# Kernel tuning notes

Hardware: AMD Instinct MI355X
Metric: run time of the kernel (lower is better)

The kernel has to match this reference:

```python
import jax, jax.numpy as jnp
import numpy as np

BETA = 0.25

def setup_inputs() -> dict:
    key = jax.random.key(0)
    k1, k2 = jax.random.split(key)
    x = jax.random.normal(k1, (16, 32, 32, 256), dtype=jnp.float32)
    embed = jax.random.normal(k2, (256, 8192), dtype=jnp.float32)
    return {"x": x, "embed": embed}

def reference(x, embed):
    dim = embed.shape[0]
    flatten = x.reshape(-1, dim)  # [N, dim]
    # squared L2 distance to each code: ||f||^2 - 2 f.e + ||e||^2 -> [N, n_embed]
    dist = (jnp.sum(flatten * flatten, axis=1, keepdims=True)
            - 2.0 * (flatten @ embed)
            + jnp.sum(embed * embed, axis=0, keepdims=True))
    ind = jnp.argmin(dist, axis=1)  # == argmax(-dist)
    embed_ind = ind.reshape(x.shape[:-1])  # [B, H, W]
    codebook = embed.T  # [n_embed, dim]
    quantize = codebook[embed_ind]  # gather -> [B, H, W, dim]
    diff = jnp.mean((jax.lax.stop_gradient(quantize) - x) ** 2)
    commit_loss = jnp.mean((quantize - jax.lax.stop_gradient(x)) ** 2)
    diff = diff + commit_loss * BETA
    quantize = x + jax.lax.stop_gradient(quantize - x)  # straight-through
    return quantize, diff, embed_ind
```

## Files before the change

kernel.cpp:

```cpp
#include <hip/hip_runtime.h>

static constexpr int DIM   = 256;
static constexpr int NCODE = 8192;
static constexpr int NROWS = 16384;

typedef __bf16 bf16x8 __attribute__((ext_vector_type(8)));
typedef float  f32x4  __attribute__((ext_vector_type(4)));

__device__ __forceinline__ void top2_insert(float& v0, int& i0, float& v1, int& i1,
                                            float s, int si) {
    if (s < v0) { v1 = v0; i1 = i0; v0 = s; i0 = si; }
    else if (s < v1) { v1 = s; i1 = si; }
}
__device__ __forceinline__ void top2_merge(float& v0, int& i0, float& v1, int& i1,
                                           float b0, int bi0, float b1, int bi1) {
    if (b0 < v0) {
        if (b1 < v0) { v0 = b0; i0 = bi0; v1 = b1; i1 = bi1; }
        else         { v1 = v0; i1 = i0;  v0 = b0; i0 = bi0; }
    } else if (b0 < v1) { v1 = b0; i1 = bi0; }
}

__global__ __launch_bounds__(256) void prep_kernel(
    const float* __restrict__ x, const float* __restrict__ embed,
    ushort* __restrict__ xb, ushort* __restrict__ eb16,
    float* __restrict__ ebT32, float* __restrict__ e2)
{
    __shared__ float tile[64][65];
    const int b = blockIdx.x;
    const int t = threadIdx.x;

    if (b < 2048) {
        int i = b * 256 + t;
        const float4* xp = (const float4*)x + (size_t)i * 2;
        float4 a = xp[0], v = xp[1];
        bf16x8 o;
        o[0] = (__bf16)a.x; o[1] = (__bf16)a.y; o[2] = (__bf16)a.z; o[3] = (__bf16)a.w;
        o[4] = (__bf16)v.x; o[5] = (__bf16)v.y; o[6] = (__bf16)v.z; o[7] = (__bf16)v.w;
        ((bf16x8*)xb)[i] = o;
    } else if (b < 2560) {
        const int eb = b - 2048;
        const int c00 = (eb & 127) * 64;
        const int k0  = (eb >> 7) * 64;
        const int tc  = t & 63, tr4 = t >> 6;
        #pragma unroll
        for (int i = 0; i < 16; ++i) {
            int r = i * 4 + tr4;
            tile[r][tc] = embed[(size_t)(k0 + r) * NCODE + c00 + tc];
        }
        __syncthreads();
        const int cl = t >> 2;
        const int kq = t & 3;
        float vals[16];
        #pragma unroll
        for (int j = 0; j < 16; ++j) vals[j] = tile[kq * 16 + j][cl];
        float* d32 = ebT32 + (size_t)(c00 + cl) * DIM + k0 + kq * 16;
        #pragma unroll
        for (int j = 0; j < 4; ++j)
            *(float4*)(d32 + j * 4) = make_float4(vals[j*4], vals[j*4+1],
                                                  vals[j*4+2], vals[j*4+3]);
        bf16x8 h0, h1;
        #pragma unroll
        for (int j = 0; j < 8; ++j) { h0[j] = (__bf16)vals[j]; h1[j] = (__bf16)vals[8 + j]; }
        ushort* d16 = eb16 + (size_t)(c00 + cl) * DIM + k0 + kq * 16;
        *(bf16x8*)d16 = h0;
        *(bf16x8*)(d16 + 8) = h1;
    } else {
        int j = (b - 2560) * 256 + t;
        float s = 0.f;
        for (int k = 0; k < DIM; ++k) {
            float v = embed[(size_t)k * NCODE + j];
            s = __fadd_rn(s, __fmul_rn(v, v));
        }
        e2[j] = s;
    }
}

__global__ __launch_bounds__(512, 1) void gemm_top2_kernel(
    const ushort* __restrict__ xb,
    const ushort* __restrict__ eb,
    const float* __restrict__ e2g,
    uint2* __restrict__ scratch)
{
    __shared__ ushort Bs[32768];
    __shared__ ushort As[2][16384];
    __shared__ uint4  ldsM[4][64];

    const int t     = threadIdx.x;
    const int chunk = blockIdx.x >> 2;
    const int rg    = blockIdx.x & 3;
    const int c0    = chunk * 128;
    const int rowbase = rg * 4096;

    const int wid = t >> 6, lane = t & 63;
    const int wr  = wid >> 2, wc = wid & 3;
    const int lr  = lane & 15, g = lane >> 4;

    {
        const char* bb = (const char*)(eb + (size_t)c0 * DIM);
        uint4 breg[8];
        #pragma unroll
        for (int i = 0; i < 8; ++i)
            breg[i] = *(const uint4*)(bb + i * 8192 + t * 16);
        #pragma unroll
        for (int i = 0; i < 8; ++i) {
            int o = i * 8192 + t * 16;
            int row = o >> 9, col = o & 511;
            *(uint4*)((char*)Bs + row * 512 + (col ^ ((row & 7) << 4))) = breg[i];
        }
        const char* ab = (const char*)(xb + (size_t)rowbase * DIM);
        uint4 areg[4];
        #pragma unroll
        for (int i = 0; i < 4; ++i)
            areg[i] = *(const uint4*)(ab + i * 8192 + t * 16);
        #pragma unroll
        for (int i = 0; i < 4; ++i) {
            int o = i * 8192 + t * 16;
            int row = o >> 9, col = o & 511;
            *(uint4*)((char*)As[0] + row * 512 + (col ^ ((row & 7) << 4))) = areg[i];
        }
    }
    __syncthreads();

    float e2v[2];
    #pragma unroll
    for (int fc = 0; fc < 2; ++fc) e2v[fc] = e2g[c0 + wc * 32 + fc * 16 + lr];

    int cur = 0;
    for (int tt = 0; tt < 64; ++tt) {
        uint4 areg[4];
        if (tt < 63) {
            const char* ab = (const char*)(xb + (size_t)(rowbase + (tt + 1) * 64) * DIM);
            #pragma unroll
            for (int i = 0; i < 4; ++i)
                areg[i] = *(const uint4*)(ab + i * 8192 + t * 16);
        }

        f32x4 acc[2][2];
        #pragma unroll
        for (int a = 0; a < 2; ++a)
            #pragma unroll
            for (int b2 = 0; b2 < 2; ++b2) acc[a][b2] = (f32x4){0.f, 0.f, 0.f, 0.f};

        const char* Ab = (const char*)As[cur];
        const char* Bb = (const char*)Bs;
        #pragma unroll
        for (int ks = 0; ks < 8; ++ks) {
            bf16x8 af[2], bfr[2];
            #pragma unroll
            for (int fr = 0; fr < 2; ++fr) {
                int row = wr * 32 + fr * 16 + lr;
                int col = (ks * 64 + g * 16) ^ ((row & 7) << 4);
                af[fr] = *(const bf16x8*)(Ab + row * 512 + col);
            }
            #pragma unroll
            for (int fc = 0; fc < 2; ++fc) {
                int code = wc * 32 + fc * 16 + lr;
                int col  = (ks * 64 + g * 16) ^ ((code & 7) << 4);
                bfr[fc] = *(const bf16x8*)(Bb + code * 512 + col);
            }
            #pragma unroll
            for (int fr = 0; fr < 2; ++fr)
                #pragma unroll
                for (int fc = 0; fc < 2; ++fc)
                    acc[fr][fc] = __builtin_amdgcn_mfma_f32_16x16x32_bf16(
                        af[fr], bfr[fc], acc[fr][fc], 0, 0, 0);
        }

        #pragma unroll
        for (int fr = 0; fr < 2; ++fr) {
            #pragma unroll
            for (int reg = 0; reg < 4; ++reg) {
                float v0 = __builtin_inff(), v1 = __builtin_inff();
                int   i0 = -1, i1 = -1;
                #pragma unroll
                for (int fc = 0; fc < 2; ++fc) {
                    float sv = __builtin_fmaf(-2.f, acc[fr][fc][reg], e2v[fc]);
                    top2_insert(v0, i0, v1, i1, sv, c0 + wc * 32 + fc * 16 + lr);
                }
                #pragma unroll
                for (int m = 1; m < 16; m <<= 1) {
                    float b0 = __shfl_xor(v0, m), b1 = __shfl_xor(v1, m);
                    int  bi0 = __shfl_xor(i0, m), bi1 = __shfl_xor(i1, m);
                    top2_merge(v0, i0, v1, i1, b0, bi0, b1, bi1);
                }
                if (lr == 0)
                    ldsM[wc][wr * 32 + fr * 16 + g * 4 + reg] =
                        make_uint4(__float_as_uint(v0), (unsigned)i0,
                                   __float_as_uint(v1), (unsigned)i1);
            }
        }
        __syncthreads();

        if (t < 64) {
            uint4 E = ldsM[0][t];
            float v0 = __uint_as_float(E.x), v1 = __uint_as_float(E.z);
            int   i0 = (int)E.y,             i1 = (int)E.w;
            #pragma unroll
            for (int k = 1; k < 4; ++k) {
                uint4 F = ldsM[k][t];
                top2_merge(v0, i0, v1, i1, __uint_as_float(F.x), (int)F.y,
                           __uint_as_float(F.z), (int)F.w);
            }
            float delta = v1 - v0;
            unsigned dq = (unsigned)min(63, (int)(delta * 32.f));
            unsigned w2 = (unsigned)i0 | ((unsigned)i1 << 13) | (dq << 26);
            scratch[(size_t)chunk * NROWS + rowbase + tt * 64 + t] =
                make_uint2(__float_as_uint(v0), w2);
        }

        if (tt < 63) {
            #pragma unroll
            for (int i = 0; i < 4; ++i) {
                int o = i * 8192 + t * 16;
                int row = o >> 9, col = o & 511;
                *(uint4*)((char*)As[cur ^ 1] + row * 512 + (col ^ ((row & 7) << 4))) = areg[i];
            }
        }
        __syncthreads();
        cur ^= 1;
    }
}

__global__ __launch_bounds__(256) void finalize_kernel(
    const uint2* __restrict__ scratch, const float* __restrict__ x,
    const float* __restrict__ ebT32, const float* __restrict__ e2g,
    float* __restrict__ quant, float* __restrict__ diff, float* __restrict__ ind)
{
    __shared__ float    wmin[4][64];
    __shared__ float    thr[64];
    __shared__ unsigned cnt[64];
    __shared__ unsigned cand[64][12];
    __shared__ unsigned bestIdx[64];
    __shared__ float    partial[4];

    const int t  = threadIdx.x;
    const int w  = t >> 6, l = t & 63;
    const int R0 = blockIdx.x * 64;

    if (t < 64) cnt[t] = 0;

    float m = __builtin_inff();
    #pragma unroll 4
    for (int i = 0; i < 16; ++i) {
        uint2 e = scratch[(size_t)(w * 16 + i) * NROWS + R0 + l];
        m = fminf(m, __uint_as_float(e.x));
    }
    wmin[w][l] = m;
    __syncthreads();
    if (t < 64)
        thr[t] = fminf(fminf(wmin[0][t], wmin[1][t]),
                       fminf(wmin[2][t], wmin[3][t])) + 1.0f;
    __syncthreads();

    const float th = thr[l];
    for (int i = 0; i < 16; ++i) {
        uint2 e = scratch[(size_t)(w * 16 + i) * NROWS + R0 + l];
        float v0 = __uint_as_float(e.x);
        if (v0 <= th) {
            unsigned s = atomicAdd(&cnt[l], 1u);
            if (s < 12) cand[l][s] = e.y & 8191u;
        }
        float v1lo = v0 + (float)((e.y >> 26) & 63u) * 0.03125f;
        if (v1lo <= th) {
            unsigned s = atomicAdd(&cnt[l], 1u);
            if (s < 12) cand[l][s] = (e.y >> 13) & 8191u;
        }
    }
    __syncthreads();

    const int rl = l >> 2, slot = l & 3;
    const int rrow = R0 + w * 16 + rl;
    const int cn = min((int)cnt[w * 16 + rl], 12);
    float best = __builtin_inff();
    unsigned bidx = 0xFFFFFFFFu;
    for (int s = slot; s < cn; s += 4) {
        unsigned idx = cand[w * 16 + rl][s];
        const float* xr = x + (size_t)rrow * DIM;
        const float* er = ebT32 + (size_t)idx * DIM;
        float f2 = 0.f, dot = 0.f;
        for (int k = 0; k < DIM; ++k) {
            float xv = xr[k];
            f2  = __fadd_rn(f2, __fmul_rn(xv, xv));
            dot = __builtin_fmaf(xv, er[k], dot);
        }
        float d = __fadd_rn(__builtin_fmaf(-2.f, dot, f2), e2g[idx]);
        if (d < best || (d == best && idx < bidx)) { best = d; bidx = idx; }
    }
    #pragma unroll
    for (int mm = 1; mm < 4; mm <<= 1) {
        float    od = __shfl_xor(best, mm);
        unsigned oi = (unsigned)__shfl_xor((int)bidx, mm);
        if (od < best || (od == best && oi < bidx)) { best = od; bidx = oi; }
    }
    if (slot == 0) bestIdx[w * 16 + rl] = bidx;
    __syncthreads();

    float accv = 0.f;
    for (int r = 0; r < 64; ++r) {
        const int row2 = R0 + r;
        const unsigned idx = bestIdx[r];
        float xv = x[(size_t)row2 * DIM + t];
        float q  = ebT32[(size_t)idx * DIM + t];
        float dq = __fsub_rn(q, xv);
        quant[(size_t)row2 * DIM + t] = __fadd_rn(xv, dq);
        accv += __fmul_rn(dq, dq);
    }
    #pragma unroll
    for (int off = 32; off >= 1; off >>= 1) accv += __shfl_down(accv, off);
    if (l == 0) partial[w] = accv;
    __syncthreads();
    if (t == 0) {
        float s = (partial[0] + partial[1]) + (partial[2] + partial[3]);
        atomicAdd(diff, s * (1.25f / 4194304.f));
    }
    if (t < 64) ind[R0 + t] = (float)bestIdx[t];
}

extern "C" void kernel_launch(void* const* d_in, const int* in_sizes, int n_in,
                              void* d_out, int out_size, void* d_ws, size_t ws_size,
                              hipStream_t stream)
{
    const float* x     = (const float*)d_in[0];
    const float* embed = (const float*)d_in[1];

    float* out   = (float*)d_out;
    float* quant = out;
    float* diff  = out + 4194304;
    float* ind   = out + 4194305;

    ushort* xb = (ushort*)quant;

    char* w = (char*)d_ws;
    ushort* eb16    = (ushort*)(w);
    float*  ebT32   = (float*) (w + 4194304);
    float*  e2      = (float*) (w + 12582912);
    uint2*  scratch = (uint2*) (w + 12615680);

    prep_kernel<<<2592, 256, 0, stream>>>(x, embed, xb, eb16, ebT32, e2);
    gemm_top2_kernel<<<256, 512, 0, stream>>>(xb, eb16, e2, scratch);
    hipMemsetAsync(diff, 0, sizeof(float), stream);
    finalize_kernel<<<256, 256, 0, stream>>>(scratch, x, ebT32, e2, quant, diff, ind);
}
```

Baseline: 648.5 us.

## Hold codebook fragments in registers and swap MFMA operands to simplify top-2 reduction

Each wave now loads its codebook (B) fragments into registers once, before the row loop, so B is no longer re-read from LDS on every tile. The MFMA operands are swapped so codes land along the per-lane register dimension. This lets each lane do a local top-2 over 8 values and then needs only two cross-lane shuffle stages instead of four per register. The LDS layout for A and B is changed to a k-group-major XOR swizzle. The cost is higher VGPR use from holding 16 bf16x8 fragments per lane.

```diff
diff --git a/kernel.cpp b/kernel.cpp
--- a/kernel.cpp
+++ b/kernel.cpp
@@ -85,10 +85,10 @@
     __shared__ ushort As[2][16384];
     __shared__ uint4  ldsM[4][64];
 
-    const int t     = threadIdx.x;
-    const int chunk = blockIdx.x >> 2;
-    const int rg    = blockIdx.x & 3;
-    const int c0    = chunk * 128;
+    const int t       = threadIdx.x;
+    const int chunk   = blockIdx.x >> 2;
+    const int rg      = blockIdx.x & 3;
+    const int c0      = chunk * 128;
     const int rowbase = rg * 4096;
 
     const int wid = t >> 6, lane = t & 63;
@@ -101,93 +101,102 @@
         #pragma unroll
         for (int i = 0; i < 8; ++i)
             breg[i] = *(const uint4*)(bb + i * 8192 + t * 16);
+        const char* ab = (const char*)(xb + (size_t)rowbase * DIM);
+        uint4 areg[4];
+        #pragma unroll
+        for (int i = 0; i < 4; ++i)
+            areg[i] = *(const uint4*)(ab + i * 8192 + t * 16);
         #pragma unroll
         for (int i = 0; i < 8; ++i) {
             int o = i * 8192 + t * 16;
-            int row = o >> 9, col = o & 511;
-            *(uint4*)((char*)Bs + row * 512 + (col ^ ((row & 7) << 4))) = breg[i];
-        }
-        const char* ab = (const char*)(xb + (size_t)rowbase * DIM);
-        uint4 areg[4];
-        #pragma unroll
-        for (int i = 0; i < 4; ++i)
-            areg[i] = *(const uint4*)(ab + i * 8192 + t * 16);
+            int code = o >> 9, kg = (o >> 4) & 31;
+            *(uint4*)((char*)Bs + kg * 2048 + (((code ^ kg) & 127) << 4)) = breg[i];
+        }
         #pragma unroll
         for (int i = 0; i < 4; ++i) {
             int o = i * 8192 + t * 16;
-            int row = o >> 9, col = o & 511;
-            *(uint4*)((char*)As[0] + row * 512 + (col ^ ((row & 7) << 4))) = areg[i];
-        }
-    }
-    __syncthreads();
-
-    float e2v[2];
+            int row = o >> 9, kg = (o >> 4) & 31;
+            *(uint4*)((char*)As[0] + kg * 1024 + (((row ^ kg) & 63) << 4)) = areg[i];
+        }
+    }
+    __syncthreads();
+
+    bf16x8 bq[2][8];
     #pragma unroll
-    for (int fc = 0; fc < 2; ++fc) e2v[fc] = e2g[c0 + wc * 32 + fc * 16 + lr];
+    for (int cf = 0; cf < 2; ++cf) {
+        #pragma unroll
+        for (int ks = 0; ks < 8; ++ks) {
+            int code = wc * 32 + cf * 16 + lr;
+            int kg   = ks * 4 + g;
+            bq[cf][ks] = *(const bf16x8*)((char*)Bs + kg * 2048 +
+                                          (((code ^ kg) & 127) << 4));
+        }
+    }
+
+    float e2v[2][4];
+    #pragma unroll
+    for (int cf = 0; cf < 2; ++cf)
+        #pragma unroll
+        for (int reg = 0; reg < 4; ++reg)
+            e2v[cf][reg] = e2g[c0 + wc * 32 + cf * 16 + g * 4 + reg];
 
     int cur = 0;
     for (int tt = 0; tt < 64; ++tt) {
-        uint4 areg[4];
+        uint4 nreg[4];
         if (tt < 63) {
-            const char* ab = (const char*)(xb + (size_t)(rowbase + (tt + 1) * 64) * DIM);
+            const char* an = (const char*)(xb + (size_t)(rowbase + (tt + 1) * 64) * DIM);
             #pragma unroll
             for (int i = 0; i < 4; ++i)
-                areg[i] = *(const uint4*)(ab + i * 8192 + t * 16);
+                nreg[i] = *(const uint4*)(an + i * 8192 + t * 16);
         }
 
         f32x4 acc[2][2];
         #pragma unroll
-        for (int a = 0; a < 2; ++a)
-            #pragma unroll
-            for (int b2 = 0; b2 < 2; ++b2) acc[a][b2] = (f32x4){0.f, 0.f, 0.f, 0.f};
+        for (int cf = 0; cf < 2; ++cf)
+            #pragma unroll
+            for (int rf = 0; rf < 2; ++rf) acc[cf][rf] = (f32x4){0.f, 0.f, 0.f, 0.f};
 
         const char* Ab = (const char*)As[cur];
-        const char* Bb = (const char*)Bs;
         #pragma unroll
         for (int ks = 0; ks < 8; ++ks) {
-            bf16x8 af[2], bfr[2];
-            #pragma unroll
-            for (int fr = 0; fr < 2; ++fr) {
-                int row = wr * 32 + fr * 16 + lr;
-                int col = (ks * 64 + g * 16) ^ ((row & 7) << 4);
-                af[fr] = *(const bf16x8*)(Ab + row * 512 + col);
-            }
-            #pragma unroll
-            for (int fc = 0; fc < 2; ++fc) {
-                int code = wc * 32 + fc * 16 + lr;
-                int col  = (ks * 64 + g * 16) ^ ((code & 7) << 4);
-                bfr[fc] = *(const bf16x8*)(Bb + code * 512 + col);
-            }
-            #pragma unroll
-            for (int fr = 0; fr < 2; ++fr)
+            bf16x8 af[2];
+            #pragma unroll
+            for (int rf = 0; rf < 2; ++rf) {
+                int row = wr * 32 + rf * 16 + lr;
+                int kg  = ks * 4 + g;
+                af[rf] = *(const bf16x8*)(Ab + kg * 1024 + (((row ^ kg) & 63) << 4));
+            }
+            #pragma unroll
+            for (int cf = 0; cf < 2; ++cf)
                 #pragma unroll
-                for (int fc = 0; fc < 2; ++fc)
-                    acc[fr][fc] = __builtin_amdgcn_mfma_f32_16x16x32_bf16(
-                        af[fr], bfr[fc], acc[fr][fc], 0, 0, 0);
-        }
-
-        #pragma unroll
-        for (int fr = 0; fr < 2; ++fr) {
-            #pragma unroll
-            for (int reg = 0; reg < 4; ++reg) {
-                float v0 = __builtin_inff(), v1 = __builtin_inff();
-                int   i0 = -1, i1 = -1;
+                for (int rf = 0; rf < 2; ++rf)
+                    acc[cf][rf] = __builtin_amdgcn_mfma_f32_16x16x32_bf16(
+                        bq[cf][ks], af[rf], acc[cf][rf], 0, 0, 0);
+        }
+
+        #pragma unroll
+        for (int rf = 0; rf < 2; ++rf) {
+            float v0 = __builtin_inff(), v1 = __builtin_inff();
+            int   i0 = -1, i1 = -1;
+            #pragma unroll
+            for (int cf = 0; cf < 2; ++cf) {
                 #pragma unroll
-                for (int fc = 0; fc < 2; ++fc) {
-                    float sv = __builtin_fmaf(-2.f, acc[fr][fc][reg], e2v[fc]);
-                    top2_insert(v0, i0, v1, i1, sv, c0 + wc * 32 + fc * 16 + lr);
+                for (int reg = 0; reg < 4; ++reg) {
+                    float sv = __builtin_fmaf(-2.f, acc[cf][rf][reg], e2v[cf][reg]);
+                    top2_insert(v0, i0, v1, i1, sv,
+                                c0 + wc * 32 + cf * 16 + g * 4 + reg);
                 }
-                #pragma unroll
-                for (int m = 1; m < 16; m <<= 1) {
-                    float b0 = __shfl_xor(v0, m), b1 = __shfl_xor(v1, m);
-                    int  bi0 = __shfl_xor(i0, m), bi1 = __shfl_xor(i1, m);
-                    top2_merge(v0, i0, v1, i1, b0, bi0, b1, bi1);
-                }
-                if (lr == 0)
-                    ldsM[wc][wr * 32 + fr * 16 + g * 4 + reg] =
-                        make_uint4(__float_as_uint(v0), (unsigned)i0,
-                                   __float_as_uint(v1), (unsigned)i1);
-            }
+            }
+            #pragma unroll
+            for (int m = 16; m <= 32; m <<= 1) {
+                float b0 = __shfl_xor(v0, m), b1 = __shfl_xor(v1, m);
+                int  bi0 = __shfl_xor(i0, m), bi1 = __shfl_xor(i1, m);
+                top2_merge(v0, i0, v1, i1, b0, bi0, b1, bi1);
+            }
+            if (g == 0)
+                ldsM[wc][wr * 32 + rf * 16 + lr] =
+                    make_uint4(__float_as_uint(v0), (unsigned)i0,
+                               __float_as_uint(v1), (unsigned)i1);
         }
         __syncthreads();
 
@@ -212,8 +221,9 @@
             #pragma unroll
             for (int i = 0; i < 4; ++i) {
                 int o = i * 8192 + t * 16;
-                int row = o >> 9, col = o & 511;
-                *(uint4*)((char*)As[cur ^ 1] + row * 512 + (col ^ ((row & 7) << 4))) = areg[i];
+                int row = o >> 9, kg = (o >> 4) & 31;
+                *(uint4*)((char*)As[cur ^ 1] + kg * 1024 +
+                          (((row ^ kg) & 63) << 4)) = nreg[i];
             }
         }
         __syncthreads();
```

Result: slower. 706.1 us (+8.9%).
